# Optimization experiments

Hardware: AMD Instinct MI355X
Metric: run time of the kernel (lower is better)

Reference implementation:

```python
import jax, jax.numpy as jnp
import numpy as np

B, N, K = 1, 8192, 32
C_S, C_Z, C_H, H, PQ, PV = 384, 128, 16, 12, 4, 8
CZ4 = C_Z // 4
INF, EPS = 1e5, 1e-8
SOFTPLUS_INV_1 = 0.541324854612918


def _lin(key, i, o):
    return jax.random.normal(key, (i, o), jnp.float32) / np.sqrt(i)


def setup_inputs() -> dict:
    key = jax.random.key(0)
    ks = jax.random.split(key, 20)
    inp = {}
    inp["s"] = jax.random.normal(ks[0], (B, N, C_S), jnp.float32)
    inp["z"] = jax.random.normal(ks[1], (B, N, K, C_Z), jnp.float32)
    inp["edge_index"] = jax.random.randint(ks[2], (B, N, K), 0, N)
    m = jax.random.normal(ks[3], (B, N, 3, 3), jnp.float32)
    q, _ = jnp.linalg.qr(m)  # random orthonormal frames
    inp["rot"] = q
    inp["trans"] = 10.0 * jax.random.normal(ks[4], (B, N, 3), jnp.float32)
    inp["mask"] = jnp.ones((B, N), jnp.float32)
    hc = C_H * H
    inp["w_q"] = _lin(ks[5], C_S, hc); inp["b_q"] = jnp.zeros((hc,), jnp.float32)
    inp["w_kv"] = _lin(ks[6], C_S, 2 * hc); inp["b_kv"] = jnp.zeros((2 * hc,), jnp.float32)
    hpq = H * PQ * 3
    inp["w_qp"] = _lin(ks[7], C_S, hpq); inp["b_qp"] = jnp.zeros((hpq,), jnp.float32)
    hpkv = H * (PQ + PV) * 3
    inp["w_kvp"] = _lin(ks[8], C_S, hpkv); inp["b_kvp"] = jnp.zeros((hpkv,), jnp.float32)
    inp["w_b"] = _lin(ks[9], C_Z, H); inp["b_b"] = jnp.zeros((H,), jnp.float32)
    inp["w_dz"] = _lin(ks[10], C_Z, CZ4); inp["b_dz"] = jnp.zeros((CZ4,), jnp.float32)
    inp["head_weights"] = jnp.full((H,), SOFTPLUS_INV_1, jnp.float32)
    cat_dim = H * (CZ4 + C_H + PV * 4)
    inp["w_out"] = _lin(ks[11], cat_dim, C_S); inp["b_out"] = jnp.zeros((C_S,), jnp.float32)
    return inp


def reference(s, z, edge_index, rot, trans, mask,
              w_q, b_q, w_kv, b_kv, w_qp, b_qp, w_kvp, b_kvp,
              w_b, b_b, w_dz, b_dz, head_weights, w_out, b_out):
    gather = jax.vmap(lambda tab, idx: tab[idx])  # per-batch gather along N

    # scalar q/k/v
    q = (s @ w_q + b_q).reshape(B, N, H, C_H)
    kv = (s @ w_kv + b_kv).reshape(B, N, H, 2 * C_H)
    kv_g = gather(kv, edge_index)                      # [B,N,K,H,2C]
    k_g, v_g = kv_g[..., :C_H], kv_g[..., C_H:]

    # point q/k/v in global frame: layout is 3 stacked chunks (x,y,z)
    def to_pts(x):
        x = x.reshape(B, N, 3, -1).swapaxes(-1, -2)     # [B,N,H*P,3]
        return jnp.einsum('bnij,bnmj->bnmi', rot, x) + trans[:, :, None, :]

    q_pts = to_pts(s @ w_qp + b_qp).reshape(B, N, H, PQ, 3)
    kv_pts = to_pts(s @ w_kvp + b_kvp).reshape(B, N, H, PQ + PV, 3)
    kv_pts_g = gather(kv_pts, edge_index)               # [B,N,K,H,PQ+PV,3]
    k_pts_g, v_pts_g = kv_pts_g[..., :PQ, :], kv_pts_g[..., PQ:, :]

    # attention logits [B,H,N,K]
    a = jnp.einsum('bnhc,bnkhc->bhnk', q, k_g) * np.sqrt(1.0 / (3 * C_H))
    b_pair = z @ w_b + b_b                              # [B,N,K,H]
    a = a + np.sqrt(1.0 / 3) * jnp.transpose(b_pair, (0, 3, 1, 2))

    disp = q_pts[:, :, None] - k_pts_g                  # [B,N,K,H,PQ,3]
    pt_att = jnp.sum(disp * disp, axis=-1)              # [B,N,K,H,PQ]
    hw = jax.nn.softplus(head_weights) * np.sqrt(1.0 / (3 * (PQ * 9.0 / 2)))
    pt_att = -0.5 * jnp.sum(pt_att * hw[None, None, None, :, None], axis=-1)
    a = a + jnp.transpose(pt_att, (0, 3, 1, 2))

    edge_mask = gather(mask, edge_index)                # [B,N,K]
    a = a + (INF * (edge_mask - 1.0))[:, None]
    a = jax.nn.softmax(a, axis=-1)

    # outputs
    o = jnp.einsum('bhnk,bnkhc->bnhc', a, v_g).reshape(B, N, H * C_H)
    o_pt = jnp.einsum('bhnk,bnkhpx->bnhpx', a, v_pts_g)  # global frame
    o_pt = jnp.einsum('bnji,bnhpj->bnhpi', rot, o_pt - trans[:, :, None, None, :])
    o_pt_norm = jnp.sqrt(jnp.sum(o_pt * o_pt, axis=-1) + EPS).reshape(B, N, H * PV)
    o_pt = o_pt.reshape(B, N, H * PV, 3)

    pair_z = z @ w_dz + b_dz                            # [B,N,K,CZ4]
    o_pair = jnp.einsum('bhnk,bnkc->bnhc', a, pair_z).reshape(B, N, H * CZ4)

    cat = jnp.concatenate([o, o_pt[..., 0], o_pt[..., 1], o_pt[..., 2],
                           o_pt_norm, o_pair], axis=-1)
    return cat @ w_out + b_out
```

## Files before the change

### kernel.cpp

```cpp
#include <hip/hip_runtime.h>
#include <hip/hip_bf16.h>
#include <math.h>

#define N_NODES 8192
#define KNN 32

typedef unsigned short ushort_t;
typedef ushort_t ushort8 __attribute__((ext_vector_type(8)));
typedef ushort_t ushort4v __attribute__((ext_vector_type(4)));
typedef short short8v __attribute__((ext_vector_type(8)));
typedef float f32x4 __attribute__((ext_vector_type(4)));

static __device__ __forceinline__ float b2f(ushort_t u) {
    union { float f; unsigned int i; } v; v.i = ((unsigned int)u) << 16; return v.f;
}
static __device__ __forceinline__ ushort_t f2b(float f) {
    __hip_bfloat16 h = __float2bfloat16(f);
    return *(ushort_t*)&h;
}

#define N_WALLT (1152 * 384)
#define N_WCATT (64 * 128)
#define N_WOUTT (384 * 960)
__global__ void build_weights(
    const float* __restrict__ wq,  const float* __restrict__ bq,
    const float* __restrict__ wkv, const float* __restrict__ bkv,
    const float* __restrict__ wqp, const float* __restrict__ bqp,
    const float* __restrict__ wkvp,const float* __restrict__ bkvp,
    const float* __restrict__ wb,  const float* __restrict__ bb,
    const float* __restrict__ wdz, const float* __restrict__ bdz,
    const float* __restrict__ wout,
    ushort_t* __restrict__ WallT, float* __restrict__ ball,
    ushort_t* __restrict__ WcatT, float* __restrict__ bcat,
    ushort_t* __restrict__ WoutT)
{
    int t = blockIdx.x * 256 + threadIdx.x;
    if (t < N_WALLT) {
        const int p = t / 384, k = t % 384;
        float v;
        if      (p < 192) v = wq  [k * 192 + p];
        else if (p < 576) v = wkv [k * 384 + (p - 192)];
        else if (p < 720) v = wqp [k * 144 + (p - 576)];
        else              v = wkvp[k * 432 + (p - 720)];
        WallT[t] = f2b(v);
    } else if (t < N_WALLT + N_WCATT) {
        const int u = t - N_WALLT;
        const int j = u >> 7, c = u & 127;
        float v = (j < 12) ? wb[c * 12 + j] : (j < 44 ? wdz[c * 32 + (j - 12)] : 0.0f);
        WcatT[u] = f2b(v);
    } else if (t < N_WALLT + N_WCATT + N_WOUTT) {
        const int u = t - N_WALLT - N_WCATT;
        const int p = u / 960, k = u % 960;
        WoutT[u] = f2b(wout[k * 384 + p]);
    } else {
        const int u = t - N_WALLT - N_WCATT - N_WOUTT;
        if (u < 1152) {
            float v;
            if      (u < 192)  v = bq[u];
            else if (u < 576)  v = bkv[u - 192];
            else if (u < 720)  v = bqp[u - 576];
            else               v = bkvp[u - 720];
            ball[u] = v;
        } else if (u < 1152 + 44) {
            const int w = u - 1152;
            bcat[w] = (w < 12) ? bb[w] : bdz[w - 12];
        }
    }
}
#define BW_TOTAL (N_WALLT + N_WCATT + N_WOUTT + 1152 + 44)

__global__ __launch_bounds__(256) void proj_fused(
    const float* __restrict__ S, const ushort_t* __restrict__ WallT,
    const float* __restrict__ ball,
    ushort_t* __restrict__ qb, ushort_t* __restrict__ kg,
    ushort_t* __restrict__ vg, float* __restrict__ praw,
    const float* __restrict__ Z, const ushort_t* __restrict__ WcT,
    const float* __restrict__ bc, ushort_t* __restrict__ zph)
{
    __shared__ ushort_t As[128][40];
    __shared__ ushort_t Bs[128][40];

    const int tid  = threadIdx.x;
    const int wave = tid >> 6;
    const int lane = tid & 63;
    const int m16 = lane & 15;
    const int kof = (lane >> 4) * 8;

    if (blockIdx.x < 4096) {
        const int row0 = blockIdx.x * 64;
        const int wm = (wave >> 1) * 32;
        const int wn = (wave & 1) * 32;
        const int a_row = tid >> 2;
        const int a_kq  = (tid & 3) * 8;

        f32x4 acc[2][2];
#pragma unroll
        for (int i = 0; i < 2; ++i)
#pragma unroll
            for (int j = 0; j < 2; ++j) acc[i][j] = (f32x4)0.0f;

        for (int k0 = 0; k0 < 128; k0 += 32) {
            {
                const float* ap = Z + (size_t)(row0 + a_row) * 128 + (k0 + a_kq);
                float4 v0 = *(const float4*)(ap);
                float4 v1 = *(const float4*)(ap + 4);
                ushort8 u;
                u[0] = f2b(v0.x); u[1] = f2b(v0.y); u[2] = f2b(v0.z); u[3] = f2b(v0.w);
                u[4] = f2b(v1.x); u[5] = f2b(v1.y); u[6] = f2b(v1.z); u[7] = f2b(v1.w);
                *(ushort8*)&As[a_row][a_kq] = u;
            }
            *(ushort8*)&Bs[a_row][a_kq] =
                *(const ushort8*)(WcT + (size_t)a_row * 128 + (k0 + a_kq));
            __syncthreads();

            short8v a[2], b[2];
#pragma unroll
            for (int mb = 0; mb < 2; ++mb)
                a[mb] = *(const short8v*)&As[wm + mb * 16 + m16][kof];
#pragma unroll
            for (int nb = 0; nb < 2; ++nb)
                b[nb] = *(const short8v*)&Bs[wn + nb * 16 + m16][kof];
#pragma unroll
            for (int mb = 0; mb < 2; ++mb)
#pragma unroll
                for (int nb = 0; nb < 2; ++nb)
                    acc[mb][nb] = __builtin_amdgcn_mfma_f32_16x16x32_bf16(
                        a[mb], b[nb], acc[mb][nb], 0, 0, 0);
            __syncthreads();
        }

        const int r_base = row0 + wm + (lane >> 4) * 4;
#pragma unroll
        for (int nb = 0; nb < 2; ++nb) {
            const int col = wn + nb * 16 + m16;
            if (col >= 44) continue;
            const float bv = bc[col];
#pragma unroll
            for (int mb = 0; mb < 2; ++mb) {
#pragma unroll
                for (int r = 0; r < 4; ++r) {
                    zph[(size_t)(r_base + mb * 16 + r) * 48 + col] =
                        f2b(acc[mb][nb][r] + bv);
                }
            }
        }
    } else {
        const int id   = blockIdx.x - 4096;
        const int ncol = 9;
        const int xcd  = id & 7;
        const int qq   = id >> 3;
        const int row0 = ((qq / ncol) * 8 + xcd) * 128;
        const int col0 = (qq % ncol) * 128;
        const int K    = 384;

        const int wm = (wave >> 1) * 64;
        const int wn = (wave & 1) * 64;
        const int a_row = tid >> 1;
        const int a_kq  = (tid & 1) * 16;

        f32x4 acc[4][4];
#pragma unroll
        for (int i = 0; i < 4; ++i)
#pragma unroll
            for (int j = 0; j < 4; ++j) acc[i][j] = (f32x4)0.0f;

        for (int k0 = 0; k0 < K; k0 += 32) {
            {
                const float* ap = S + (size_t)(row0 + a_row) * K + (k0 + a_kq);
                float4 v0 = *(const float4*)(ap);
                float4 v1 = *(const float4*)(ap + 4);
                float4 v2 = *(const float4*)(ap + 8);
                float4 v3 = *(const float4*)(ap + 12);
                ushort8 u0, u1;
                u0[0] = f2b(v0.x); u0[1] = f2b(v0.y); u0[2] = f2b(v0.z); u0[3] = f2b(v0.w);
                u0[4] = f2b(v1.x); u0[5] = f2b(v1.y); u0[6] = f2b(v1.z); u0[7] = f2b(v1.w);
                u1[0] = f2b(v2.x); u1[1] = f2b(v2.y); u1[2] = f2b(v2.z); u1[3] = f2b(v2.w);
                u1[4] = f2b(v3.x); u1[5] = f2b(v3.y); u1[6] = f2b(v3.z); u1[7] = f2b(v3.w);
                *(ushort8*)&As[a_row][a_kq]     = u0;
                *(ushort8*)&As[a_row][a_kq + 8] = u1;
            }
            {
                const ushort_t* wp = WallT + (size_t)(col0 + a_row) * K + (k0 + a_kq);
                *(ushort8*)&Bs[a_row][a_kq]     = *(const ushort8*)(wp);
                *(ushort8*)&Bs[a_row][a_kq + 8] = *(const ushort8*)(wp + 8);
            }
            __syncthreads();

            short8v a[4], b[4];
#pragma unroll
            for (int mb = 0; mb < 4; ++mb)
                a[mb] = *(const short8v*)&As[wm + mb * 16 + m16][kof];
#pragma unroll
            for (int nb = 0; nb < 4; ++nb)
                b[nb] = *(const short8v*)&Bs[wn + nb * 16 + m16][kof];
#pragma unroll
            for (int mb = 0; mb < 4; ++mb)
#pragma unroll
                for (int nb = 0; nb < 4; ++nb)
                    acc[mb][nb] = __builtin_amdgcn_mfma_f32_16x16x32_bf16(
                        a[mb], b[nb], acc[mb][nb], 0, 0, 0);
            __syncthreads();
        }

        const int r_base = row0 + wm + (lane >> 4) * 4;
#pragma unroll
        for (int nb = 0; nb < 4; ++nb) {
            const int col = col0 + wn + nb * 16 + m16;
            const float bv = ball[col];
#pragma unroll
            for (int mb = 0; mb < 4; ++mb) {
#pragma unroll
                for (int r = 0; r < 4; ++r) {
                    const int row = r_base + mb * 16 + r;
                    const float v = acc[mb][nb][r] + bv;
                    if (col < 192) {
                        qb[(size_t)row * 192 + col] = f2b(v);
                    } else if (col < 576) {
                        const int u = col - 192, h = u >> 5, c = u & 31;
                        if (c < 16) kg[(size_t)row * 480 + h * 16 + c] = f2b(v);
                        else        vg[(size_t)row * 480 + h * 16 + (c - 16)] = f2b(v);
                    } else {
                        praw[(size_t)row * 576 + (col - 576)] = v;
                    }
                }
            }
        }
    }
}

__global__ __launch_bounds__(256) void gemm_out(
    const ushort_t* __restrict__ A, const ushort_t* __restrict__ WT,
    const float* __restrict__ bias, float* __restrict__ C)
{
    __shared__ ushort_t As[64][40];
    __shared__ ushort_t Bs[64][40];

    const int tid  = threadIdx.x;
    const int ncol = 6;
    const int id   = blockIdx.x;
    const int xcd  = id & 7;
    const int qq   = id >> 3;
    const int row0 = ((qq / ncol) * 8 + xcd) * 64;
    const int col0 = (qq % ncol) * 64;
    const int K = 960, P = 384;

    const int wave = tid >> 6;
    const int lane = tid & 63;
    const int wm = (wave >> 1) * 32;
    const int wn = (wave & 1) * 32;
    const int m16 = lane & 15;
    const int kof = (lane >> 4) * 8;

    const int a_row = tid >> 2;
    const int a_kq  = (tid & 3) * 8;

    f32x4 acc[2][2];
#pragma unroll
    for (int i = 0; i < 2; ++i)
#pragma unroll
        for (int j = 0; j < 2; ++j) acc[i][j] = (f32x4)0.0f;

    for (int k0 = 0; k0 < K; k0 += 32) {
        *(ushort8*)&As[a_row][a_kq] =
            *(const ushort8*)(A + (size_t)(row0 + a_row) * K + (k0 + a_kq));
        *(ushort8*)&Bs[a_row][a_kq] =
            *(const ushort8*)(WT + (size_t)(col0 + a_row) * K + (k0 + a_kq));
        __syncthreads();

        short8v a[2], b[2];
#pragma unroll
        for (int mb = 0; mb < 2; ++mb)
            a[mb] = *(const short8v*)&As[wm + mb * 16 + m16][kof];
#pragma unroll
        for (int nb = 0; nb < 2; ++nb)
            b[nb] = *(const short8v*)&Bs[wn + nb * 16 + m16][kof];
#pragma unroll
        for (int mb = 0; mb < 2; ++mb)
#pragma unroll
            for (int nb = 0; nb < 2; ++nb)
                acc[mb][nb] = __builtin_amdgcn_mfma_f32_16x16x32_bf16(
                    a[mb], b[nb], acc[mb][nb], 0, 0, 0);
        __syncthreads();
    }

    const int r_base = row0 + wm + (lane >> 4) * 4;
#pragma unroll
    for (int nb = 0; nb < 2; ++nb) {
        const int col = col0 + wn + nb * 16 + m16;
        const float bv = bias[col];
#pragma unroll
        for (int mb = 0; mb < 2; ++mb) {
#pragma unroll
            for (int r = 0; r < 4; ++r) {
                C[(size_t)(r_base + mb * 16 + r) * P + col] = acc[mb][nb][r] + bv;
            }
        }
    }
}

__global__ void prep_pts(const float* __restrict__ praw,
                         const float* __restrict__ rot,
                         const float* __restrict__ trans,
                         float* __restrict__ q_pts,
                         ushort_t* __restrict__ kg,
                         ushort_t* __restrict__ vg)
{
    int t = blockIdx.x * 256 + threadIdx.x;
    if (t >= N_NODES * 192) return;
    const int n = t / 192;
    const int m = t % 192;
    const float* row = praw + (size_t)n * 576;
    const float* R  = rot + n * 9;
    const float* tr = trans + n * 3;
    float X, Y, Z;
    if (m < 48) { X = row[m];      Y = row[48 + m];  Z = row[96 + m]; }
    else { const int pt = m - 48;
           X = row[144 + pt]; Y = row[288 + pt]; Z = row[432 + pt]; }
    const float gx = R[0] * X + R[1] * Y + R[2] * Z + tr[0];
    const float gy = R[3] * X + R[4] * Y + R[5] * Z + tr[1];
    const float gz = R[6] * X + R[7] * Y + R[8] * Z + tr[2];
    if (m < 48) {
        const int h = m >> 2, p = m & 3;
        float* dst = q_pts + (size_t)n * 144 + h * 12 + p * 3;
        dst[0] = gx; dst[1] = gy; dst[2] = gz;
    } else {
        const int pt = m - 48, h = pt / 12, p = pt % 12;
        if (p < 4) {
            float* dst = (float*)(kg + (size_t)n * 480 + 192) + h * 12 + p * 3;
            dst[0] = gx; dst[1] = gy; dst[2] = gz;
        } else {
            ushort_t* dst = vg + (size_t)n * 480 + 192 + h * 24 + (p - 4) * 3;
            dst[0] = f2b(gx); dst[1] = f2b(gy); dst[2] = f2b(gz);
        }
    }
}

__global__ __launch_bounds__(256, 8) void attn_kernel(
    const ushort_t* __restrict__ qb,
    const ushort_t* __restrict__ kg,
    const ushort_t* __restrict__ vg,
    const float* __restrict__ q_pts,
    const ushort_t* __restrict__ zph,
    const int*   __restrict__ eidx,
    const float* __restrict__ mask,
    const float* __restrict__ rot,
    const float* __restrict__ trans,
    const float* __restrict__ head_weights,
    ushort_t* __restrict__ catb)
{
    const int n   = blockIdx.x;
    const int tid = threadIdx.x;

    __shared__ ushort_t zp[32][48];
    __shared__ float q_s[192];
    __shared__ float qp_s[144];
    __shared__ float a_s[12][33];
    __shared__ float opt[288];
    __shared__ int   idx_s[32];
    __shared__ float madd_s[32];
    __shared__ float R_s[9];
    __shared__ float t_s[3];
    __shared__ float hw_s[12];

    for (int i = tid; i < 192; i += 256) q_s[i]  = b2f(qb[(size_t)n * 192 + i]);
    for (int i = tid; i < 144; i += 256) qp_s[i] = q_pts[(size_t)n * 144 + i];
    if (tid < 32) {
        const int ix = eidx[n * 32 + tid];
        idx_s[tid]  = ix;
        madd_s[tid] = 100000.0f * (mask[ix] - 1.0f);
    }
    if (tid >= 32 && tid < 41) R_s[tid - 32]  = rot[n * 9 + (tid - 32)];
    if (tid >= 41 && tid < 44) t_s[tid - 41]  = trans[n * 3 + (tid - 41)];
    if (tid >= 44 && tid < 56) {
        float x = head_weights[tid - 44];
        hw_s[tid - 44] = log1pf(__expf(x)) * 0.13608276348795434f;
    }
    if (tid < 192) {
        const int r = tid / 6, sg = tid % 6;
        *(ushort8*)&zp[r][sg * 8] =
            *(const ushort8*)(zph + ((size_t)n * 32 + r) * 48 + sg * 8);
    }
    __syncthreads();

    {
        int j, h0, h1;
        if (tid < 128) { j = tid & 31; h0 = tid >> 5;        h1 = h0 + 8; }
        else           { int u = tid - 128; j = u & 31; h0 = 4 + (u >> 5); h1 = -1; }
        const int ix = idx_s[j];
        const ushort_t* kbase = kg + (size_t)ix * 480;
        const float* kptf = (const float*)(kbase + 192);
        const float  madd = madd_s[j];

        ushort8 ka0 = *(const ushort8*)(kbase + h0 * 16);
        ushort8 ka1 = *(const ushort8*)(kbase + h0 * 16 + 8);
        float4 pa0 = *(const float4*)(kptf + h0 * 12);
        float4 pa1 = *(const float4*)(kptf + h0 * 12 + 4);
        float4 pa2 = *(const float4*)(kptf + h0 * 12 + 8);
        ushort8 kb0, kb1; float4 pb0, pb1, pb2;
        if (h1 >= 0) {
            kb0 = *(const ushort8*)(kbase + h1 * 16);
            kb1 = *(const ushort8*)(kbase + h1 * 16 + 8);
            pb0 = *(const float4*)(kptf + h1 * 12);
            pb1 = *(const float4*)(kptf + h1 * 12 + 4);
            pb2 = *(const float4*)(kptf + h1 * 12 + 8);
        }

        {
            const float* qh = q_s + h0 * 16;
            float dot = 0.0f;
#pragma unroll
            for (int c = 0; c < 8; ++c) dot += qh[c] * b2f(ka0[c]);
#pragma unroll
            for (int c = 0; c < 8; ++c) dot += qh[8 + c] * b2f(ka1[c]);
            const float* qp = qp_s + h0 * 12;
            float d, pt = 0.0f;
            d = qp[0]  - pa0.x; pt += d * d;  d = qp[1]  - pa0.y; pt += d * d;
            d = qp[2]  - pa0.z; pt += d * d;  d = qp[3]  - pa0.w; pt += d * d;
            d = qp[4]  - pa1.x; pt += d * d;  d = qp[5]  - pa1.y; pt += d * d;
            d = qp[6]  - pa1.z; pt += d * d;  d = qp[7]  - pa1.w; pt += d * d;
            d = qp[8]  - pa2.x; pt += d * d;  d = qp[9]  - pa2.y; pt += d * d;
            d = qp[10] - pa2.z; pt += d * d;  d = qp[11] - pa2.w; pt += d * d;
            a_s[h0][j] = 0.14433756729740643f * dot
                       + 0.5773502691896258f * b2f(zp[j][h0])
                       - 0.5f * hw_s[h0] * pt + madd;
        }
        if (h1 >= 0) {
            const float* qh = q_s + h1 * 16;
            float dot = 0.0f;
#pragma unroll
            for (int c = 0; c < 8; ++c) dot += qh[c] * b2f(kb0[c]);
#pragma unroll
            for (int c = 0; c < 8; ++c) dot += qh[8 + c] * b2f(kb1[c]);
            const float* qp = qp_s + h1 * 12;
            float d, pt = 0.0f;
            d = qp[0]  - pb0.x; pt += d * d;  d = qp[1]  - pb0.y; pt += d * d;
            d = qp[2]  - pb0.z; pt += d * d;  d = qp[3]  - pb0.w; pt += d * d;
            d = qp[4]  - pb1.x; pt += d * d;  d = qp[5]  - pb1.y; pt += d * d;
            d = qp[6]  - pb1.z; pt += d * d;  d = qp[7]  - pb1.w; pt += d * d;
            d = qp[8]  - pb2.x; pt += d * d;  d = qp[9]  - pb2.y; pt += d * d;
            d = qp[10] - pb2.z; pt += d * d;  d = qp[11] - pb2.w; pt += d * d;
            a_s[h1][j] = 0.14433756729740643f * dot
                       + 0.5773502691896258f * b2f(zp[j][h1])
                       - 0.5f * hw_s[h1] * pt + madd;
        }
    }
    __syncthreads();

    if (tid < 96) {
        const int h = tid >> 3, g = tid & 7;
        float a0 = a_s[h][g * 4 + 0], a1 = a_s[h][g * 4 + 1];
        float a2 = a_s[h][g * 4 + 2], a3 = a_s[h][g * 4 + 3];
        float m = fmaxf(fmaxf(a0, a1), fmaxf(a2, a3));
        m = fmaxf(m, __shfl_xor(m, 1)); m = fmaxf(m, __shfl_xor(m, 2));
        m = fmaxf(m, __shfl_xor(m, 4));
        float e0 = __expf(a0 - m), e1 = __expf(a1 - m);
        float e2 = __expf(a2 - m), e3 = __expf(a3 - m);
        float s = e0 + e1 + e2 + e3;
        s += __shfl_xor(s, 1); s += __shfl_xor(s, 2); s += __shfl_xor(s, 4);
        const float inv = 1.0f / s;
        a_s[h][g * 4 + 0] = e0 * inv; a_s[h][g * 4 + 1] = e1 * inv;
        a_s[h][g * 4 + 2] = e2 * inv; a_s[h][g * 4 + 3] = e3 * inv;
    }
    __syncthreads();

    ushort_t* catn = catb + (size_t)n * 960;
    if (tid < 48) {
        const int h = tid >> 2, cq = tid & 3;
        const int boff = h * 16 + cq * 4;
        float s0 = 0, s1 = 0, s2 = 0, s3 = 0;
#pragma unroll 8
        for (int j = 0; j < 32; ++j) {
            const float aj = a_s[h][j];
            ushort4v v = *(const ushort4v*)(vg + (size_t)idx_s[j] * 480 + boff);
            s0 += aj * b2f(v[0]); s1 += aj * b2f(v[1]);
            s2 += aj * b2f(v[2]); s3 += aj * b2f(v[3]);
        }
        ushort4v o = { f2b(s0), f2b(s1), f2b(s2), f2b(s3) };
        *(ushort4v*)&catn[h * 16 + cq * 4] = o;
    } else if (tid < 120) {
        const int u = tid - 48;
        const int h = u / 6, rq = u % 6;
        const int boff = 192 + h * 24 + rq * 4;
        float s0 = 0, s1 = 0, s2 = 0, s3 = 0;
#pragma unroll 8
        for (int j = 0; j < 32; ++j) {
            const float aj = a_s[h][j];
            ushort4v v = *(const ushort4v*)(vg + (size_t)idx_s[j] * 480 + boff);
            s0 += aj * b2f(v[0]); s1 += aj * b2f(v[1]);
            s2 += aj * b2f(v[2]); s3 += aj * b2f(v[3]);
        }
        float* od = opt + h * 24 + rq * 4;
        od[0] = s0; od[1] = s1; od[2] = s2; od[3] = s3;
    } else if (tid < 216) {
        const int u = tid - 120;
        const int h = u >> 3, cq = u & 7;
        float s0 = 0, s1 = 0, s2 = 0, s3 = 0;
#pragma unroll 8
        for (int j = 0; j < 32; ++j) {
            const float aj = a_s[h][j];
            ushort4v zv = *(const ushort4v*)&zp[j][12 + cq * 4];
            s0 += aj * b2f(zv[0]); s1 += aj * b2f(zv[1]);
            s2 += aj * b2f(zv[2]); s3 += aj * b2f(zv[3]);
        }
        ushort4v o = { f2b(s0), f2b(s1), f2b(s2), f2b(s3) };
        *(ushort4v*)&catn[576 + h * 32 + cq * 4] = o;
    }
    __syncthreads();

    if (tid < 96) {
        const int h = tid >> 3, p = tid & 7;
        const float* ob = opt + h * 24 + p * 3;
        float gx = ob[0] - t_s[0];
        float gy = ob[1] - t_s[1];
        float gz = ob[2] - t_s[2];
        float lx = R_s[0] * gx + R_s[3] * gy + R_s[6] * gz;
        float ly = R_s[1] * gx + R_s[4] * gy + R_s[7] * gz;
        float lz = R_s[2] * gx + R_s[5] * gy + R_s[8] * gz;
        const int hp = h * 8 + p;
        catn[192 + hp] = f2b(lx);
        catn[288 + hp] = f2b(ly);
        catn[384 + hp] = f2b(lz);
        catn[480 + hp] = f2b(sqrtf(lx * lx + ly * ly + lz * lz + 1e-8f));
    }
}

extern "C" void kernel_launch(void* const* d_in, const int* in_sizes, int n_in,
                              void* d_out, int out_size, void* d_ws, size_t ws_size,
                              hipStream_t stream)
{
    const float* s     = (const float*)d_in[0];
    const float* z     = (const float*)d_in[1];
    const int*   eidx  = (const int*)  d_in[2];
    const float* rot   = (const float*)d_in[3];
    const float* trans = (const float*)d_in[4];
    const float* mask  = (const float*)d_in[5];
    const float* w_q   = (const float*)d_in[6];
    const float* b_q   = (const float*)d_in[7];
    const float* w_kv  = (const float*)d_in[8];
    const float* b_kv  = (const float*)d_in[9];
    const float* w_qp  = (const float*)d_in[10];
    const float* b_qp  = (const float*)d_in[11];
    const float* w_kvp = (const float*)d_in[12];
    const float* b_kvp = (const float*)d_in[13];
    const float* w_b   = (const float*)d_in[14];
    const float* b_b   = (const float*)d_in[15];
    const float* w_dz  = (const float*)d_in[16];
    const float* b_dz  = (const float*)d_in[17];
    const float* hw    = (const float*)d_in[18];
    const float* w_out = (const float*)d_in[19];
    const float* b_out = (const float*)d_in[20];
    float* out = (float*)d_out;

    float* ws = (float*)d_ws;
    size_t off = 0;
    ushort_t* qb    = (ushort_t*)(ws + off); off += (size_t)N_NODES * 96;
    ushort_t* kg    = (ushort_t*)(ws + off); off += (size_t)N_NODES * 240;
    ushort_t* vg    = (ushort_t*)(ws + off); off += (size_t)N_NODES * 240;
    float* praw     = ws + off;              off += (size_t)N_NODES * 576;
    float* q_pts    = ws + off;              off += (size_t)N_NODES * 144;
    ushort_t* zph   = (ushort_t*)(ws + off); off += (size_t)N_NODES * KNN * 24;
    ushort_t* catb  = (ushort_t*)(ws + off); off += (size_t)N_NODES * 480;
    ushort_t* WallT = (ushort_t*)(ws + off); off += N_WALLT / 2;
    float* ball     = ws + off;              off += 1152;
    ushort_t* WcatT = (ushort_t*)(ws + off); off += N_WCATT / 2;
    float* bcat     = ws + off;              off += 44;
    ushort_t* WoutT = (ushort_t*)(ws + off); off += N_WOUTT / 2;

    build_weights<<<(BW_TOTAL + 255) / 256, 256, 0, stream>>>(
        w_q, b_q, w_kv, b_kv, w_qp, b_qp, w_kvp, b_kvp,
        w_b, b_b, w_dz, b_dz, w_out, WallT, ball, WcatT, bcat, WoutT);

    proj_fused<<<4096 + 576, 256, 0, stream>>>(
        s, WallT, ball, qb, kg, vg, praw, z, WcatT, bcat, zph);

    prep_pts<<<(N_NODES * 192 + 255) / 256, 256, 0, stream>>>(
        praw, rot, trans, q_pts, kg, vg);

    attn_kernel<<<N_NODES, 256, 0, stream>>>(
        qb, kg, vg, q_pts, zph, eidx, mask, rot, trans, hw, catb);

    gemm_out<<<(N_NODES / 64) * 6, 256, 0, stream>>>(catb, WoutT, b_out, out);
}
```

Baseline: 175.2 us.

## Split fused projection kernel into separate s-projection and z-projection kernels

The single fused kernel, which dispatched z-projection and s-projection blocks by block index, is replaced with two dedicated kernels. The z-projection kernel now allocates only its own smaller shared-memory tiles and is launched after point preparation. The aim is to lower per-block LDS and register footprint for the many small z blocks and to remove divergent kernel code. The cost is an extra launch and the loss of concurrency between the two GEMMs within one grid.

```diff
diff --git a/kernel.cpp b/kernel.cpp
--- a/kernel.cpp
+++ b/kernel.cpp
@@ -69,160 +69,170 @@
 }
 #define BW_TOTAL (N_WALLT + N_WCATT + N_WOUTT + 1152 + 44)
 
-__global__ __launch_bounds__(256) void proj_fused(
-    const float* __restrict__ S, const ushort_t* __restrict__ WallT,
-    const float* __restrict__ ball,
+__global__ __launch_bounds__(256) void gemm_sproj(
+    const float* __restrict__ S, const ushort_t* __restrict__ WT,
+    const float* __restrict__ bias,
     ushort_t* __restrict__ qb, ushort_t* __restrict__ kg,
-    ushort_t* __restrict__ vg, float* __restrict__ praw,
+    ushort_t* __restrict__ vg, float* __restrict__ praw)
+{
+    __shared__ ushort_t As[128][40];
+    __shared__ ushort_t Bs[128][40];
+
+    const int tid  = threadIdx.x;
+    const int ncol = 9;
+    const int id   = blockIdx.x;
+    const int xcd  = id & 7;
+    const int qq   = id >> 3;
+    const int row0 = ((qq / ncol) * 8 + xcd) * 128;
+    const int col0 = (qq % ncol) * 128;
+    const int K    = 384;
+
+    const int wave = tid >> 6;
+    const int lane = tid & 63;
+    const int wm = (wave >> 1) * 64;
+    const int wn = (wave & 1) * 64;
+    const int m16 = lane & 15;
+    const int kof = (lane >> 4) * 8;
+
+    const int a_row = tid >> 1;
+    const int a_kq  = (tid & 1) * 16;
+
+    f32x4 acc[4][4];
+#pragma unroll
+    for (int i = 0; i < 4; ++i)
+#pragma unroll
+        for (int j = 0; j < 4; ++j) acc[i][j] = (f32x4)0.0f;
+
+    for (int k0 = 0; k0 < K; k0 += 32) {
+        {
+            const float* ap = S + (size_t)(row0 + a_row) * K + (k0 + a_kq);
+            float4 v0 = *(const float4*)(ap);
+            float4 v1 = *(const float4*)(ap + 4);
+            float4 v2 = *(const float4*)(ap + 8);
+            float4 v3 = *(const float4*)(ap + 12);
+            ushort8 u0, u1;
+            u0[0] = f2b(v0.x); u0[1] = f2b(v0.y); u0[2] = f2b(v0.z); u0[3] = f2b(v0.w);
+            u0[4] = f2b(v1.x); u0[5] = f2b(v1.y); u0[6] = f2b(v1.z); u0[7] = f2b(v1.w);
+            u1[0] = f2b(v2.x); u1[1] = f2b(v2.y); u1[2] = f2b(v2.z); u1[3] = f2b(v2.w);
+            u1[4] = f2b(v3.x); u1[5] = f2b(v3.y); u1[6] = f2b(v3.z); u1[7] = f2b(v3.w);
+            *(ushort8*)&As[a_row][a_kq]     = u0;
+            *(ushort8*)&As[a_row][a_kq + 8] = u1;
+        }
+        {
+            const ushort_t* wp = WT + (size_t)(col0 + a_row) * K + (k0 + a_kq);
+            *(ushort8*)&Bs[a_row][a_kq]     = *(const ushort8*)(wp);
+            *(ushort8*)&Bs[a_row][a_kq + 8] = *(const ushort8*)(wp + 8);
+        }
+        __syncthreads();
+
+        short8v a[4], b[4];
+#pragma unroll
+        for (int mb = 0; mb < 4; ++mb)
+            a[mb] = *(const short8v*)&As[wm + mb * 16 + m16][kof];
+#pragma unroll
+        for (int nb = 0; nb < 4; ++nb)
+            b[nb] = *(const short8v*)&Bs[wn + nb * 16 + m16][kof];
+#pragma unroll
+        for (int mb = 0; mb < 4; ++mb)
+#pragma unroll
+            for (int nb = 0; nb < 4; ++nb)
+                acc[mb][nb] = __builtin_amdgcn_mfma_f32_16x16x32_bf16(
+                    a[mb], b[nb], acc[mb][nb], 0, 0, 0);
+        __syncthreads();
+    }
+
+    const int r_base = row0 + wm + (lane >> 4) * 4;
+#pragma unroll
+    for (int nb = 0; nb < 4; ++nb) {
+        const int col = col0 + wn + nb * 16 + m16;
+        const float bv = bias[col];
+#pragma unroll
+        for (int mb = 0; mb < 4; ++mb) {
+#pragma unroll
+            for (int r = 0; r < 4; ++r) {
+                const int row = r_base + mb * 16 + r;
+                const float v = acc[mb][nb][r] + bv;
+                if (col < 192) {
+                    qb[(size_t)row * 192 + col] = f2b(v);
+                } else if (col < 576) {
+                    const int u = col - 192, h = u >> 5, c = u & 31;
+                    if (c < 16) kg[(size_t)row * 480 + h * 16 + c] = f2b(v);
+                    else        vg[(size_t)row * 480 + h * 16 + (c - 16)] = f2b(v);
+                } else {
+                    praw[(size_t)row * 576 + (col - 576)] = v;
+                }
+            }
+        }
+    }
+}
+
+__global__ __launch_bounds__(256) void gemm_zproj(
     const float* __restrict__ Z, const ushort_t* __restrict__ WcT,
     const float* __restrict__ bc, ushort_t* __restrict__ zph)
 {
-    __shared__ ushort_t As[128][40];
-    __shared__ ushort_t Bs[128][40];
+    __shared__ ushort_t As[64][40];
+    __shared__ ushort_t Bs[64][40];
 
     const int tid  = threadIdx.x;
+    const int row0 = blockIdx.x * 64;
+
     const int wave = tid >> 6;
     const int lane = tid & 63;
+    const int wm = (wave >> 1) * 32;
+    const int wn = (wave & 1) * 32;
     const int m16 = lane & 15;
     const int kof = (lane >> 4) * 8;
 
-    if (blockIdx.x < 4096) {
-        const int row0 = blockIdx.x * 64;
-        const int wm = (wave >> 1) * 32;
-        const int wn = (wave & 1) * 32;
-        const int a_row = tid >> 2;
-        const int a_kq  = (tid & 3) * 8;
-
-        f32x4 acc[2][2];
-#pragma unroll
-        for (int i = 0; i < 2; ++i)
-#pragma unroll
-            for (int j = 0; j < 2; ++j) acc[i][j] = (f32x4)0.0f;
-
-        for (int k0 = 0; k0 < 128; k0 += 32) {
-            {
-                const float* ap = Z + (size_t)(row0 + a_row) * 128 + (k0 + a_kq);
-                float4 v0 = *(const float4*)(ap);
-                float4 v1 = *(const float4*)(ap + 4);
-                ushort8 u;
-                u[0] = f2b(v0.x); u[1] = f2b(v0.y); u[2] = f2b(v0.z); u[3] = f2b(v0.w);
-                u[4] = f2b(v1.x); u[5] = f2b(v1.y); u[6] = f2b(v1.z); u[7] = f2b(v1.w);
-                *(ushort8*)&As[a_row][a_kq] = u;
-            }
-            *(ushort8*)&Bs[a_row][a_kq] =
-                *(const ushort8*)(WcT + (size_t)a_row * 128 + (k0 + a_kq));
-            __syncthreads();
-
-            short8v a[2], b[2];
-#pragma unroll
-            for (int mb = 0; mb < 2; ++mb)
-                a[mb] = *(const short8v*)&As[wm + mb * 16 + m16][kof];
+    const int a_row = tid >> 2;
+    const int a_kq  = (tid & 3) * 8;
+
+    f32x4 acc[2][2];
+#pragma unroll
+    for (int i = 0; i < 2; ++i)
+#pragma unroll
+        for (int j = 0; j < 2; ++j) acc[i][j] = (f32x4)0.0f;
+
+    for (int k0 = 0; k0 < 128; k0 += 32) {
+        {
+            const float* ap = Z + (size_t)(row0 + a_row) * 128 + (k0 + a_kq);
+            float4 v0 = *(const float4*)(ap);
+            float4 v1 = *(const float4*)(ap + 4);
+            ushort8 u;
+            u[0] = f2b(v0.x); u[1] = f2b(v0.y); u[2] = f2b(v0.z); u[3] = f2b(v0.w);
+            u[4] = f2b(v1.x); u[5] = f2b(v1.y); u[6] = f2b(v1.z); u[7] = f2b(v1.w);
+            *(ushort8*)&As[a_row][a_kq] = u;
+        }
+        *(ushort8*)&Bs[a_row][a_kq] =
+            *(const ushort8*)(WcT + (size_t)a_row * 128 + (k0 + a_kq));
+        __syncthreads();
+
+        short8v a[2], b[2];
+#pragma unroll
+        for (int mb = 0; mb < 2; ++mb)
+            a[mb] = *(const short8v*)&As[wm + mb * 16 + m16][kof];
+#pragma unroll
+        for (int nb = 0; nb < 2; ++nb)
+            b[nb] = *(const short8v*)&Bs[wn + nb * 16 + m16][kof];
+#pragma unroll
+        for (int mb = 0; mb < 2; ++mb)
 #pragma unroll
             for (int nb = 0; nb < 2; ++nb)
-                b[nb] = *(const short8v*)&Bs[wn + nb * 16 + m16][kof];
-#pragma unroll
-            for (int mb = 0; mb < 2; ++mb)
-#pragma unroll
-                for (int nb = 0; nb < 2; ++nb)
-                    acc[mb][nb] = __builtin_amdgcn_mfma_f32_16x16x32_bf16(
-                        a[mb], b[nb], acc[mb][nb], 0, 0, 0);
-            __syncthreads();
-        }
-
-        const int r_base = row0 + wm + (lane >> 4) * 4;
-#pragma unroll
-        for (int nb = 0; nb < 2; ++nb) {
-            const int col = wn + nb * 16 + m16;
-            if (col >= 44) continue;
-            const float bv = bc[col];
-#pragma unroll
-            for (int mb = 0; mb < 2; ++mb) {
-#pragma unroll
-                for (int r = 0; r < 4; ++r) {
-                    zph[(size_t)(r_base + mb * 16 + r) * 48 + col] =
-                        f2b(acc[mb][nb][r] + bv);
-                }
-            }
-        }
-    } else {
-        const int id   = blockIdx.x - 4096;
-        const int ncol = 9;
-        const int xcd  = id & 7;
-        const int qq   = id >> 3;
-        const int row0 = ((qq / ncol) * 8 + xcd) * 128;
-        const int col0 = (qq % ncol) * 128;
-        const int K    = 384;
-
-        const int wm = (wave >> 1) * 64;
-        const int wn = (wave & 1) * 64;
-        const int a_row = tid >> 1;
-        const int a_kq  = (tid & 1) * 16;
-
-        f32x4 acc[4][4];
-#pragma unroll
-        for (int i = 0; i < 4; ++i)
-#pragma unroll
-            for (int j = 0; j < 4; ++j) acc[i][j] = (f32x4)0.0f;
-
-        for (int k0 = 0; k0 < K; k0 += 32) {
-            {
-                const float* ap = S + (size_t)(row0 + a_row) * K + (k0 + a_kq);
-                float4 v0 = *(const float4*)(ap);
-                float4 v1 = *(const float4*)(ap + 4);
-                float4 v2 = *(const float4*)(ap + 8);
-                float4 v3 = *(const float4*)(ap + 12);
-                ushort8 u0, u1;
-                u0[0] = f2b(v0.x); u0[1] = f2b(v0.y); u0[2] = f2b(v0.z); u0[3] = f2b(v0.w);
-                u0[4] = f2b(v1.x); u0[5] = f2b(v1.y); u0[6] = f2b(v1.z); u0[7] = f2b(v1.w);
-                u1[0] = f2b(v2.x); u1[1] = f2b(v2.y); u1[2] = f2b(v2.z); u1[3] = f2b(v2.w);
-                u1[4] = f2b(v3.x); u1[5] = f2b(v3.y); u1[6] = f2b(v3.z); u1[7] = f2b(v3.w);
-                *(ushort8*)&As[a_row][a_kq]     = u0;
-                *(ushort8*)&As[a_row][a_kq + 8] = u1;
-            }
-            {
-                const ushort_t* wp = WallT + (size_t)(col0 + a_row) * K + (k0 + a_kq);
-                *(ushort8*)&Bs[a_row][a_kq]     = *(const ushort8*)(wp);
-                *(ushort8*)&Bs[a_row][a_kq + 8] = *(const ushort8*)(wp + 8);
-            }
-            __syncthreads();
-
-            short8v a[4], b[4];
-#pragma unroll
-            for (int mb = 0; mb < 4; ++mb)
-                a[mb] = *(const short8v*)&As[wm + mb * 16 + m16][kof];
-#pragma unroll
-            for (int nb = 0; nb < 4; ++nb)
-                b[nb] = *(const short8v*)&Bs[wn + nb * 16 + m16][kof];
-#pragma unroll
-            for (int mb = 0; mb < 4; ++mb)
-#pragma unroll
-                for (int nb = 0; nb < 4; ++nb)
-                    acc[mb][nb] = __builtin_amdgcn_mfma_f32_16x16x32_bf16(
-                        a[mb], b[nb], acc[mb][nb], 0, 0, 0);
-            __syncthreads();
-        }
-
-        const int r_base = row0 + wm + (lane >> 4) * 4;
-#pragma unroll
-        for (int nb = 0; nb < 4; ++nb) {
-            const int col = col0 + wn + nb * 16 + m16;
-            const float bv = ball[col];
-#pragma unroll
-            for (int mb = 0; mb < 4; ++mb) {
-#pragma unroll
-                for (int r = 0; r < 4; ++r) {
-                    const int row = r_base + mb * 16 + r;
-                    const float v = acc[mb][nb][r] + bv;
-                    if (col < 192) {
-                        qb[(size_t)row * 192 + col] = f2b(v);
-                    } else if (col < 576) {
-                        const int u = col - 192, h = u >> 5, c = u & 31;
-                        if (c < 16) kg[(size_t)row * 480 + h * 16 + c] = f2b(v);
-                        else        vg[(size_t)row * 480 + h * 16 + (c - 16)] = f2b(v);
-                    } else {
-                        praw[(size_t)row * 576 + (col - 576)] = v;
-                    }
-                }
+                acc[mb][nb] = __builtin_amdgcn_mfma_f32_16x16x32_bf16(
+                    a[mb], b[nb], acc[mb][nb], 0, 0, 0);
+        __syncthreads();
+    }
+
+    const int r_base = row0 + wm + (lane >> 4) * 4;
+#pragma unroll
+    for (int nb = 0; nb < 2; ++nb) {
+        const int col = wn + nb * 16 + m16;
+        if (col >= 44) continue;
+        const float bv = bc[col];
+#pragma unroll
+        for (int mb = 0; mb < 2; ++mb) {
+#pragma unroll
+            for (int r = 0; r < 4; ++r) {
+                zph[(size_t)(r_base + mb * 16 + r) * 48 + col] = f2b(acc[mb][nb][r] + bv);
             }
         }
     }
@@ -570,12 +580,14 @@
         w_q, b_q, w_kv, b_kv, w_qp, b_qp, w_kvp, b_kvp,
         w_b, b_b, w_dz, b_dz, w_out, WallT, ball, WcatT, bcat, WoutT);
 
-    proj_fused<<<4096 + 576, 256, 0, stream>>>(
-        s, WallT, ball, qb, kg, vg, praw, z, WcatT, bcat, zph);
+    gemm_sproj<<<(N_NODES / 128) * 9, 256, 0, stream>>>(
+        s, WallT, ball, qb, kg, vg, praw);
 
     prep_pts<<<(N_NODES * 192 + 255) / 256, 256, 0, stream>>>(
         praw, rot, trans, q_pts, kg, vg);
 
+    gemm_zproj<<<(N_NODES * KNN) / 64, 256, 0, stream>>>(z, WcatT, bcat, zph);
+
     attn_kernel<<<N_NODES, 256, 0, stream>>>(
         qb, kg, vg, q_pts, zph, eidx, mask, rot, trans, hw, catb);
 
```

New measurement: 174.8 us. Within noise of the previous version (-0.2%).
